# Kernel tuning notes

Hardware: AMD Instinct MI355X
Metric: run time of the kernel (lower is better)

The kernel has to match this reference:

```python
import jax, jax.numpy as jnp
import numpy as np

B, L = 128, 4096
H, RH, D, K = 128, 64, 64, 512  # num_hiddens, residual_hiddens, embedding_dim, num_embeddings
BETA = 0.25  # commitment_cost


def conv1d(x, w, b=None, stride=1, pad=0):
    # x: (N, C, W); w: (O, I, K) torch layout
    y = jax.lax.conv_general_dilated(x, w, (stride,), [(pad, pad)],
                                     dimension_numbers=('NCW', 'OIW', 'NCW'))
    return y if b is None else y + b[None, :, None]


def convT1d(x, w, b=None, stride=2, pad=1):
    # torch ConvTranspose1d weight layout (in, out, k)
    k = w.shape[-1]
    w_t = jnp.flip(w, -1).transpose(1, 0, 2)  # (out, in, k)
    y = jax.lax.conv_general_dilated(x, w_t, (1,), [(k - 1 - pad, k - 1 - pad)],
                                     lhs_dilation=(stride,),
                                     dimension_numbers=('NCW', 'OIW', 'NCW'))
    return y if b is None else y + b[None, :, None]


def res_stack(x, layers):
    for w1, w2 in layers:
        h = conv1d(jax.nn.relu(x), w1, None, 1, 1)
        h = conv1d(jax.nn.relu(h), w2, None, 1, 0)
        x = x + h
    return jax.nn.relu(x)


def _forward(x, enc_w1, enc_b1, enc_w2, enc_b2, enc_w3, enc_b3,
             enc_r1a, enc_r1b, enc_r2a, enc_r2b, pre_vq_w, pre_vq_b, codebook,
             dec_w1, dec_b1, dec_r1a, dec_r1b, dec_r2a, dec_r2b,
             dec_ct1_w, dec_ct1_b, dec_ct2_w, dec_ct2_b):
    # ---- Encoder (compression_factor == 4) ----
    h = x[:, None, :]                                   # (B, 1, L)
    h = jax.nn.relu(conv1d(h, enc_w1, enc_b1, 2, 1))    # (B, H/2, L/2)
    h = jax.nn.relu(conv1d(h, enc_w2, enc_b2, 2, 1))    # (B, H, L/4)
    h = conv1d(h, enc_w3, enc_b3, 1, 1)
    h = res_stack(h, [(enc_r1a, enc_r1b), (enc_r2a, enc_r2b)])
    z = conv1d(h, pre_vq_w, pre_vq_b, 1, 0)             # (B, D, T)

    # ---- Vector quantization ----
    zt = z.transpose(0, 2, 1)                           # (B, T, D)
    flat = zt.reshape(-1, D)                            # (BT, D)
    dists = (jnp.sum(flat * flat, 1, keepdims=True)
             - 2.0 * flat @ codebook.T
             + jnp.sum(codebook * codebook, 1))         # (BT, K)
    idx = jnp.argmin(dists, axis=1)                     # (BT,)
    q = codebook[idx].reshape(zt.shape)                 # (B, T, D)

    e_latent = jnp.mean((jax.lax.stop_gradient(q) - zt) ** 2)
    q_latent = jnp.mean((q - jax.lax.stop_gradient(zt)) ** 2)
    loss = q_latent + BETA * e_latent
    q_st = zt + jax.lax.stop_gradient(q - zt)           # straight-through

    counts = jnp.zeros((K,), flat.dtype).at[idx].add(1.0)
    probs = counts / idx.shape[0]
    perplexity = jnp.exp(-jnp.sum(probs * jnp.log(probs + 1e-10)))

    # ---- Decoder (compression_factor == 4) ----
    hd = q_st.transpose(0, 2, 1)                        # (B, D, T)
    hd = conv1d(hd, dec_w1, dec_b1, 1, 1)               # (B, H, T)
    hd = res_stack(hd, [(dec_r1a, dec_r1b), (dec_r2a, dec_r2b)])
    hd = jax.nn.relu(convT1d(hd, dec_ct1_w, dec_ct1_b)) # (B, H/2, 2T)
    hd = convT1d(hd, dec_ct2_w, dec_ct2_b)              # (B, 1, 4T)
    recon = jnp.squeeze(hd)                             # (B, L)
    return loss, recon, perplexity


def setup_inputs() -> dict:
    key = jax.random.key(0)
    ks = jax.random.split(key, 32)
    n = lambda i, shape, s=0.05: jax.random.normal(ks[i], shape, jnp.float32) * s
    inp = {
        'x': jax.random.normal(ks[0], (B, L), jnp.float32),
        'enc_w1': n(1, (H // 2, 1, 4)), 'enc_b1': jnp.zeros((H // 2,), jnp.float32),
        'enc_w2': n(2, (H, H // 2, 4)), 'enc_b2': jnp.zeros((H,), jnp.float32),
        'enc_w3': n(3, (H, H, 3)), 'enc_b3': jnp.zeros((H,), jnp.float32),
        'enc_r1a': n(4, (RH, H, 3)), 'enc_r1b': n(5, (H, RH, 1)),
        'enc_r2a': n(6, (RH, H, 3)), 'enc_r2b': n(7, (H, RH, 1)),
        'pre_vq_w': n(8, (D, H, 1)), 'pre_vq_b': jnp.zeros((D,), jnp.float32),
        'codebook': jax.random.uniform(ks[9], (K, D), jnp.float32, -1.0 / K, 1.0 / K),
        'dec_w1': n(10, (H, D, 3)), 'dec_b1': jnp.zeros((H,), jnp.float32),
        'dec_r1a': n(11, (RH, H, 3)), 'dec_r1b': n(12, (H, RH, 1)),
        'dec_r2a': n(13, (RH, H, 3)), 'dec_r2b': n(14, (H, RH, 1)),
        'dec_ct1_w': n(15, (H, H // 2, 4)), 'dec_ct1_b': jnp.zeros((H // 2,), jnp.float32),
        'dec_ct2_w': n(16, (H // 2, 1, 4)), 'dec_ct2_b': jnp.zeros((1,), jnp.float32),
    }
    return inp


def reference(x, enc_w1, enc_b1, enc_w2, enc_b2, enc_w3, enc_b3,
              enc_r1a, enc_r1b, enc_r2a, enc_r2b, pre_vq_w, pre_vq_b, codebook,
              dec_w1, dec_b1, dec_r1a, dec_r1b, dec_r2a, dec_r2b,
              dec_ct1_w, dec_ct1_b, dec_ct2_w, dec_ct2_b):
    return _forward(x, enc_w1, enc_b1, enc_w2, enc_b2, enc_w3, enc_b3,
                    enc_r1a, enc_r1b, enc_r2a, enc_r2b, pre_vq_w, pre_vq_b, codebook,
                    dec_w1, dec_b1, dec_r1a, dec_r1b, dec_r2a, dec_r2b,
                    dec_ct1_w, dec_ct1_b, dec_ct2_w, dec_ct2_b)
```

## Files before the change

kernel.cpp:

```cpp
#include <hip/hip_runtime.h>
#include <hip/hip_bf16.h>
#include <math.h>

using bf16 = __hip_bfloat16;
typedef __attribute__((ext_vector_type(4))) float f32x4;
typedef __attribute__((ext_vector_type(8))) short s16x8;

#define MFMA16(a,b,c) __builtin_amdgcn_mfma_f32_16x16x32_bf16((a),(b),(c),0,0,0)


__device__ inline float bf2f(unsigned short u) {
    union { float f; unsigned v; } c; c.v = ((unsigned)u) << 16; return c.f;
}
__device__ inline unsigned short bfbits(float f) {
    union { bf16 h; unsigned short u; } c; c.h = __float2bfloat16(f); return c.u;
}
__device__ inline s16x8 relu8(s16x8 v) {
#pragma unroll
    for (int j = 0; j < 8; ++j)
        v[j] = (short)(((unsigned short)v[j] & 0x8000u) ? 0 : (unsigned short)v[j]);
    return v;
}

__global__ __launch_bounds__(256, 3) void encmid_k(
    const bf16* __restrict__ in, const bf16* __restrict__ w3t,
    const float* __restrict__ b3, const bf16* __restrict__ r1w1,
    const bf16* __restrict__ r1w2, const bf16* __restrict__ r2w1,
    const bf16* __restrict__ r2w2, bf16* __restrict__ out)
{
    __shared__ __align__(16) char smem[47872];
    char* sY = smem;
    char* sX = smem + 21760;
    char* sH = smem + 21760;
    const int tid = threadIdx.x;
    const int b   = blockIdx.y;
    const int l0  = blockIdx.x * 64;
    const bf16* inb = in + (size_t)b * 1024 * 128;

    for (int i = tid; i < 96 * 16; i += 256) {
        int t = i >> 4, c0 = (i & 15) * 8;
        int g = l0 - 16 + t;
        s16x8 v = {};
        if (g >= 0 && g < 1024) v = *(const s16x8*)(inb + (size_t)g * 128 + c0);
        *(s16x8*)(sX + ((t * 136 + c0) << 1)) = v;
    }
    __syncthreads();

    const int lane = tid & 63;
    const int wid  = __builtin_amdgcn_readfirstlane(tid >> 6);
    const int lr   = lane & 15;
    const int kg   = lane >> 4;
    const f32x4 zf4 = {0.f, 0.f, 0.f, 0.f};

    {
        const int co0 = wid * 32;
        f32x4 acc[2][5];
#pragma unroll
        for (int cf = 0; cf < 2; ++cf)
#pragma unroll
            for (int lf = 0; lf < 5; ++lf) acc[cf][lf] = zf4;
#pragma unroll
        for (int k = 0; k < 3; ++k) {
            const bf16* Ab = w3t + (size_t)k * 128 * 128;
#pragma unroll
            for (int ks = 0; ks < 4; ++ks) {
                s16x8 af[2];
#pragma unroll
                for (int cf = 0; cf < 2; ++cf)
                    af[cf] = *(const s16x8*)(Ab + (co0 + cf * 16 + lr) * 128 + ks * 32 + kg * 8);
                s16x8 bfr[5];
#pragma unroll
                for (int lf = 0; lf < 5; ++lf) {
                    int tx = lf * 16 + lr + 7 + k;
                    bfr[lf] = *(const s16x8*)(sX + ((tx * 136 + ks * 32 + kg * 8) << 1));
                }
#pragma unroll
                for (int cf = 0; cf < 2; ++cf)
#pragma unroll
                    for (int lf = 0; lf < 5; ++lf)
                        acc[cf][lf] = MFMA16(af[cf], bfr[lf], acc[cf][lf]);
            }
        }
        __syncthreads();
#pragma unroll
        for (int cf = 0; cf < 2; ++cf)
#pragma unroll
            for (int lf = 0; lf < 5; ++lf) {
                int row = lf * 16 + lr;
                int p   = l0 - 8 + row;
                int cb0 = co0 + cf * 16 + kg * 4;
                bool ok = (p >= 0 && p < 1024);
                float r[4];
#pragma unroll
                for (int j = 0; j < 4; ++j)
                    r[j] = ok ? (acc[cf][lf][j] + b3[cb0 + j]) : 0.f;
                uint2 pk;
                pk.x = (unsigned)bfbits(r[0]) | ((unsigned)bfbits(r[1]) << 16);
                pk.y = (unsigned)bfbits(r[2]) | ((unsigned)bfbits(r[3]) << 16);
                *(uint2*)(sY + ((row * 136 + cb0) << 1)) = pk;
            }
    }
    __syncthreads();

#pragma unroll 1
    for (int blk = 0; blk < 2; ++blk) {
        const bf16* w1 = blk ? r2w1 : r1w1;
        {
            const int co0 = wid * 16;
            f32x4 acc[5];
#pragma unroll
            for (int lf = 0; lf < 5; ++lf) acc[lf] = zf4;
#pragma unroll
            for (int k = 0; k < 3; ++k) {
                const bf16* Ab = w1 + (size_t)k * 64 * 128;
#pragma unroll
                for (int ks = 0; ks < 4; ++ks) {
                    s16x8 a = *(const s16x8*)(Ab + (co0 + lr) * 128 + ks * 32 + kg * 8);
                    s16x8 bfr[5];
#pragma unroll
                    for (int lf = 0; lf < 5; ++lf) {
                        int ry = lf * 16 + lr + k - 1;
                        ry = (ry < 0) ? 0 : (ry > 79 ? 79 : ry);
                        bfr[lf] = relu8(*(const s16x8*)(sY + ((ry * 136 + ks * 32 + kg * 8) << 1)));
                    }
#pragma unroll
                    for (int lf = 0; lf < 5; ++lf)
                        acc[lf] = MFMA16(a, bfr[lf], acc[lf]);
                }
            }
#pragma unroll
            for (int lf = 0; lf < 5; ++lf) {
                int row = lf * 16 + lr;
                int ch0 = co0 + kg * 4;
                uint2 pk;
                pk.x = (unsigned)bfbits(fmaxf(acc[lf][0], 0.f)) |
                       ((unsigned)bfbits(fmaxf(acc[lf][1], 0.f)) << 16);
                pk.y = (unsigned)bfbits(fmaxf(acc[lf][2], 0.f)) |
                       ((unsigned)bfbits(fmaxf(acc[lf][3], 0.f)) << 16);
                *(uint2*)(sH + ((row * 72 + ch0) << 1)) = pk;
            }
        }
        __syncthreads();

        if (blk == 0) {
            const int co0 = wid * 32;
            f32x4 acc[2][5];
#pragma unroll
            for (int cf = 0; cf < 2; ++cf)
#pragma unroll
                for (int lf = 0; lf < 5; ++lf) acc[cf][lf] = zf4;
#pragma unroll
            for (int ks = 0; ks < 2; ++ks) {
                s16x8 af[2];
#pragma unroll
                for (int cf = 0; cf < 2; ++cf)
                    af[cf] = *(const s16x8*)(r1w2 + (size_t)(co0 + cf * 16 + lr) * 64 + ks * 32 + kg * 8);
                s16x8 bfr[5];
#pragma unroll
                for (int lf = 0; lf < 5; ++lf) {
                    int row = lf * 16 + lr;
                    bfr[lf] = *(const s16x8*)(sH + ((row * 72 + ks * 32 + kg * 8) << 1));
                }
#pragma unroll
                for (int cf = 0; cf < 2; ++cf)
#pragma unroll
                    for (int lf = 0; lf < 5; ++lf)
                        acc[cf][lf] = MFMA16(af[cf], bfr[lf], acc[cf][lf]);
            }
#pragma unroll
            for (int cf = 0; cf < 2; ++cf)
#pragma unroll
                for (int lf = 0; lf < 5; ++lf) {
                    int row = lf * 16 + lr;
                    int p   = l0 - 8 + row;
                    int cb0 = co0 + cf * 16 + kg * 4;
                    uint2 old = *(const uint2*)(sY + ((row * 136 + cb0) << 1));
                    bool ok = (p >= 0 && p < 1024);
                    float r[4];
                    r[0] = acc[cf][lf][0] + bf2f((unsigned short)(old.x & 0xffff));
                    r[1] = acc[cf][lf][1] + bf2f((unsigned short)(old.x >> 16));
                    r[2] = acc[cf][lf][2] + bf2f((unsigned short)(old.y & 0xffff));
                    r[3] = acc[cf][lf][3] + bf2f((unsigned short)(old.y >> 16));
                    uint2 pk;
                    pk.x = ok ? ((unsigned)bfbits(r[0]) | ((unsigned)bfbits(r[1]) << 16)) : 0u;
                    pk.y = ok ? ((unsigned)bfbits(r[2]) | ((unsigned)bfbits(r[3]) << 16)) : 0u;
                    *(uint2*)(sY + ((row * 136 + cb0) << 1)) = pk;
                }
            __syncthreads();
        } else {
            const int co0 = wid * 32;
            f32x4 acc[2][4];
#pragma unroll
            for (int cf = 0; cf < 2; ++cf)
#pragma unroll
                for (int lf = 0; lf < 4; ++lf) acc[cf][lf] = zf4;
#pragma unroll
            for (int ks = 0; ks < 2; ++ks) {
                s16x8 af[2];
#pragma unroll
                for (int cf = 0; cf < 2; ++cf)
                    af[cf] = *(const s16x8*)(r2w2 + (size_t)(co0 + cf * 16 + lr) * 64 + ks * 32 + kg * 8);
                s16x8 bfr[4];
#pragma unroll
                for (int lf = 0; lf < 4; ++lf) {
                    int row = 8 + lf * 16 + lr;
                    bfr[lf] = *(const s16x8*)(sH + ((row * 72 + ks * 32 + kg * 8) << 1));
                }
#pragma unroll
                for (int cf = 0; cf < 2; ++cf)
#pragma unroll
                    for (int lf = 0; lf < 4; ++lf)
                        acc[cf][lf] = MFMA16(af[cf], bfr[lf], acc[cf][lf]);
            }
#pragma unroll
            for (int cf = 0; cf < 2; ++cf)
#pragma unroll
                for (int lf = 0; lf < 4; ++lf) {
                    int row = 8 + lf * 16 + lr;
                    int cb0 = co0 + cf * 16 + kg * 4;
                    uint2 old = *(const uint2*)(sY + ((row * 136 + cb0) << 1));
                    float r[4];
                    r[0] = fmaxf(acc[cf][lf][0] + bf2f((unsigned short)(old.x & 0xffff)), 0.f);
                    r[1] = fmaxf(acc[cf][lf][1] + bf2f((unsigned short)(old.x >> 16)), 0.f);
                    r[2] = fmaxf(acc[cf][lf][2] + bf2f((unsigned short)(old.y & 0xffff)), 0.f);
                    r[3] = fmaxf(acc[cf][lf][3] + bf2f((unsigned short)(old.y >> 16)), 0.f);
                    uint2 pk;
                    pk.x = (unsigned)bfbits(r[0]) | ((unsigned)bfbits(r[1]) << 16);
                    pk.y = (unsigned)bfbits(r[2]) | ((unsigned)bfbits(r[3]) << 16);
                    *(uint2*)(out + ((size_t)b * 1024 + l0 + lf * 16 + lr) * 128 + cb0) = pk;
                }
        }
    }
}

__global__ __launch_bounds__(256, 4) void decmid_k(
    const bf16* __restrict__ qin, const bf16* __restrict__ dw1,
    const float* __restrict__ db1, const bf16* __restrict__ r1w1,
    const bf16* __restrict__ r1w2, const bf16* __restrict__ r2w1,
    const bf16* __restrict__ r2w2, const bf16* __restrict__ ct1w,
    const float* __restrict__ ct1b, bf16* __restrict__ out)
{
    __shared__ __align__(16) char smem[35584];
    char* sY = smem;
    char* sQ = smem + 21760;
    char* sH = smem + 21760;
    const int tid = threadIdx.x;
    const int b   = blockIdx.y;
    const int l0  = blockIdx.x * 64;
    const bf16* inb = qin + (size_t)b * 1024 * 64;

    for (int i = tid; i < 96 * 8; i += 256) {
        int t = i >> 3, c0 = (i & 7) * 8;
        int g = l0 - 16 + t;
        s16x8 v = {};
        if (g >= 0 && g < 1024) v = *(const s16x8*)(inb + (size_t)g * 64 + c0);
        *(s16x8*)(sQ + ((t * 72 + c0) << 1)) = v;
    }
    __syncthreads();

    const int lane = tid & 63;
    const int wid  = __builtin_amdgcn_readfirstlane(tid >> 6);
    const int lr   = lane & 15;
    const int kg   = lane >> 4;
    const f32x4 zf4 = {0.f, 0.f, 0.f, 0.f};

    {
        const int co0 = wid * 32;
        f32x4 acc[2][5];
#pragma unroll
        for (int cf = 0; cf < 2; ++cf)
#pragma unroll
            for (int lf = 0; lf < 5; ++lf) acc[cf][lf] = zf4;
#pragma unroll
        for (int k = 0; k < 3; ++k) {
            const bf16* Ab = dw1 + (size_t)k * 128 * 64;
#pragma unroll
            for (int ks = 0; ks < 2; ++ks) {
                s16x8 af[2];
#pragma unroll
                for (int cf = 0; cf < 2; ++cf)
                    af[cf] = *(const s16x8*)(Ab + (co0 + cf * 16 + lr) * 64 + ks * 32 + kg * 8);
                s16x8 bfr[5];
#pragma unroll
                for (int lf = 0; lf < 5; ++lf) {
                    int tx = lf * 16 + lr + 7 + k;
                    bfr[lf] = *(const s16x8*)(sQ + ((tx * 72 + ks * 32 + kg * 8) << 1));
                }
#pragma unroll
                for (int cf = 0; cf < 2; ++cf)
#pragma unroll
                    for (int lf = 0; lf < 5; ++lf)
                        acc[cf][lf] = MFMA16(af[cf], bfr[lf], acc[cf][lf]);
            }
        }
        __syncthreads();
#pragma unroll
        for (int cf = 0; cf < 2; ++cf)
#pragma unroll
            for (int lf = 0; lf < 5; ++lf) {
                int row = lf * 16 + lr;
                int p   = l0 - 8 + row;
                int cb0 = co0 + cf * 16 + kg * 4;
                bool ok = (p >= 0 && p < 1024);
                float r[4];
#pragma unroll
                for (int j = 0; j < 4; ++j)
                    r[j] = ok ? (acc[cf][lf][j] + db1[cb0 + j]) : 0.f;
                uint2 pk;
                pk.x = (unsigned)bfbits(r[0]) | ((unsigned)bfbits(r[1]) << 16);
                pk.y = (unsigned)bfbits(r[2]) | ((unsigned)bfbits(r[3]) << 16);
                *(uint2*)(sY + ((row * 136 + cb0) << 1)) = pk;
            }
    }
    __syncthreads();

#pragma unroll 1
    for (int blk = 0; blk < 2; ++blk) {
        const bf16* w1 = blk ? r2w1 : r1w1;
        const bf16* w2 = blk ? r2w2 : r1w2;
        {
            const int co0 = wid * 16;
            f32x4 acc[5];
#pragma unroll
            for (int lf = 0; lf < 5; ++lf) acc[lf] = zf4;
#pragma unroll
            for (int k = 0; k < 3; ++k) {
                const bf16* Ab = w1 + (size_t)k * 64 * 128;
#pragma unroll
                for (int ks = 0; ks < 4; ++ks) {
                    s16x8 a = *(const s16x8*)(Ab + (co0 + lr) * 128 + ks * 32 + kg * 8);
                    s16x8 bfr[5];
#pragma unroll
                    for (int lf = 0; lf < 5; ++lf) {
                        int ry = lf * 16 + lr + k - 1;
                        ry = (ry < 0) ? 0 : (ry > 79 ? 79 : ry);
                        bfr[lf] = relu8(*(const s16x8*)(sY + ((ry * 136 + ks * 32 + kg * 8) << 1)));
                    }
#pragma unroll
                    for (int lf = 0; lf < 5; ++lf)
                        acc[lf] = MFMA16(a, bfr[lf], acc[lf]);
                }
            }
#pragma unroll
            for (int lf = 0; lf < 5; ++lf) {
                int row = lf * 16 + lr;
                int ch0 = co0 + kg * 4;
                uint2 pk;
                pk.x = (unsigned)bfbits(fmaxf(acc[lf][0], 0.f)) |
                       ((unsigned)bfbits(fmaxf(acc[lf][1], 0.f)) << 16);
                pk.y = (unsigned)bfbits(fmaxf(acc[lf][2], 0.f)) |
                       ((unsigned)bfbits(fmaxf(acc[lf][3], 0.f)) << 16);
                *(uint2*)(sH + ((row * 72 + ch0) << 1)) = pk;
            }
        }
        __syncthreads();
        {
            const int co0 = wid * 32;
            f32x4 acc[2][5];
#pragma unroll
            for (int cf = 0; cf < 2; ++cf)
#pragma unroll
                for (int lf = 0; lf < 5; ++lf) acc[cf][lf] = zf4;
#pragma unroll
            for (int ks = 0; ks < 2; ++ks) {
                s16x8 af[2];
#pragma unroll
                for (int cf = 0; cf < 2; ++cf)
                    af[cf] = *(const s16x8*)(w2 + (size_t)(co0 + cf * 16 + lr) * 64 + ks * 32 + kg * 8);
                s16x8 bfr[5];
#pragma unroll
                for (int lf = 0; lf < 5; ++lf) {
                    int row = lf * 16 + lr;
                    bfr[lf] = *(const s16x8*)(sH + ((row * 72 + ks * 32 + kg * 8) << 1));
                }
#pragma unroll
                for (int cf = 0; cf < 2; ++cf)
#pragma unroll
                    for (int lf = 0; lf < 5; ++lf)
                        acc[cf][lf] = MFMA16(af[cf], bfr[lf], acc[cf][lf]);
            }
#pragma unroll
            for (int cf = 0; cf < 2; ++cf)
#pragma unroll
                for (int lf = 0; lf < 5; ++lf) {
                    int row = lf * 16 + lr;
                    int p   = l0 - 8 + row;
                    int cb0 = co0 + cf * 16 + kg * 4;
                    uint2 old = *(const uint2*)(sY + ((row * 136 + cb0) << 1));
                    bool ok = (p >= 0 && p < 1024);
                    float r[4];
                    r[0] = acc[cf][lf][0] + bf2f((unsigned short)(old.x & 0xffff));
                    r[1] = acc[cf][lf][1] + bf2f((unsigned short)(old.x >> 16));
                    r[2] = acc[cf][lf][2] + bf2f((unsigned short)(old.y & 0xffff));
                    r[3] = acc[cf][lf][3] + bf2f((unsigned short)(old.y >> 16));
                    if (blk == 1)
#pragma unroll
                        for (int j = 0; j < 4; ++j) r[j] = fmaxf(r[j], 0.f);
                    uint2 pk;
                    pk.x = ok ? ((unsigned)bfbits(r[0]) | ((unsigned)bfbits(r[1]) << 16)) : 0u;
                    pk.y = ok ? ((unsigned)bfbits(r[2]) | ((unsigned)bfbits(r[3]) << 16)) : 0u;
                    *(uint2*)(sY + ((row * 136 + cb0) << 1)) = pk;
                }
        }
        __syncthreads();
    }

    {
        const int co0 = (wid & 1) * 32;
        const int mh  = wid >> 1;
        f32x4 acc[2][2][2];
#pragma unroll
        for (int g = 0; g < 2; ++g)
#pragma unroll
            for (int cf = 0; cf < 2; ++cf)
#pragma unroll
                for (int j = 0; j < 2; ++j) acc[g][cf][j] = zf4;
#pragma unroll
        for (int g = 0; g < 2; ++g)
#pragma unroll
            for (int k = 0; k < 2; ++k) {
                const bf16* Ab = ct1w + (size_t)(g * 2 + k) * 64 * 128;
                const int doff = (g == 0) ? (k - 1) : k;
#pragma unroll
                for (int ks = 0; ks < 4; ++ks) {
                    s16x8 af[2];
#pragma unroll
                    for (int cf = 0; cf < 2; ++cf)
                        af[cf] = *(const s16x8*)(Ab + (co0 + cf * 16 + lr) * 128 + ks * 32 + kg * 8);
                    s16x8 bfr[2];
#pragma unroll
                    for (int j = 0; j < 2; ++j) {
                        int ty = 8 + (mh * 2 + j) * 16 + lr + doff;
                        bfr[j] = *(const s16x8*)(sY + ((ty * 136 + ks * 32 + kg * 8) << 1));
                    }
#pragma unroll
                    for (int cf = 0; cf < 2; ++cf)
#pragma unroll
                        for (int j = 0; j < 2; ++j)
                            acc[g][cf][j] = MFMA16(af[cf], bfr[j], acc[g][cf][j]);
                }
            }
#pragma unroll
        for (int g = 0; g < 2; ++g)
#pragma unroll
            for (int cf = 0; cf < 2; ++cf)
#pragma unroll
                for (int j = 0; j < 2; ++j) {
                    int m   = (mh * 2 + j) * 16 + lr;
                    int cb0 = co0 + cf * 16 + kg * 4;
                    float r[4];
#pragma unroll
                    for (int jj = 0; jj < 4; ++jj)
                        r[jj] = fmaxf(acc[g][cf][j][jj] + ct1b[cb0 + jj], 0.f);
                    uint2 pk;
                    pk.x = (unsigned)bfbits(r[0]) | ((unsigned)bfbits(r[1]) << 16);
                    pk.y = (unsigned)bfbits(r[2]) | ((unsigned)bfbits(r[3]) << 16);
                    *(uint2*)(out + ((size_t)b * 2048 + 2 * (l0 + m) + g) * 64 + cb0) = pk;
                }
    }
}

__global__ __launch_bounds__(256) void enc12_k(
    const float* __restrict__ x, const float* __restrict__ w1,
    const float* __restrict__ b1, const bf16* __restrict__ w2t,
    const float* __restrict__ b2, bf16* __restrict__ out)
{
    __shared__ float sXf[268];
    __shared__ float sW1[256];
    __shared__ float sB1[64];
    __shared__ __align__(16) char sX[132 * 144];
    const int tid = threadIdx.x;
    const int b   = blockIdx.y;
    const int l0  = blockIdx.x * 64;
    const float* xb = x + (size_t)b * 4096;

    for (int i = tid; i < 266; i += 256) {
        int g = 4 * l0 - 3 + i;
        sXf[i] = (g >= 0 && g < 4096) ? xb[g] : 0.f;
    }
    if (tid < 256) sW1[tid] = w1[tid];
    if (tid < 64)  sB1[tid] = b1[tid];
    __syncthreads();

    for (int i = tid; i < 132 * 64; i += 256) {
        int t = i >> 6, c = i & 63;
        int p = (t < 66) ? 2 * (l0 + t) : 2 * (l0 + t - 66) - 1;
        float v = 0.f;
        if (p >= 0 && p < 2048) {
            int xi = 2 * p - 4 * l0 + 2;
            float a = sB1[c];
#pragma unroll
            for (int k = 0; k < 4; ++k) a = fmaf(sXf[xi + k], sW1[c * 4 + k], a);
            v = fmaxf(a, 0.f);
        }
        *(bf16*)(sX + ((t * 72 + c) << 1)) = __float2bfloat16(v);
    }
    __syncthreads();

    const int lane = tid & 63;
    const int wid  = __builtin_amdgcn_readfirstlane(tid >> 6);
    const int co0  = wid * 32;
    const int lr   = lane & 15;
    const int kg   = lane >> 4;

    f32x4 acc[2][4];
#pragma unroll
    for (int cf = 0; cf < 2; ++cf)
#pragma unroll
        for (int lf = 0; lf < 4; ++lf) acc[cf][lf] = (f32x4){0.f, 0.f, 0.f, 0.f};

#pragma unroll
    for (int k = 0; k < 4; ++k) {
        const int roff = (k == 0) ? 66 : (k == 1) ? 0 : (k == 2) ? 67 : 1;
        const bf16* Ab = w2t + (size_t)k * 128 * 64;
#pragma unroll
        for (int ks = 0; ks < 2; ++ks) {
            s16x8 af[2];
#pragma unroll
            for (int cf = 0; cf < 2; ++cf)
                af[cf] = *(const s16x8*)(Ab + (co0 + cf * 16 + lr) * 64 + ks * 32 + kg * 8);
            s16x8 bfr[4];
#pragma unroll
            for (int lf = 0; lf < 4; ++lf) {
                int t = roff + lf * 16 + lr;
                bfr[lf] = *(const s16x8*)(sX + ((t * 72 + ks * 32 + kg * 8) << 1));
            }
#pragma unroll
            for (int cf = 0; cf < 2; ++cf)
#pragma unroll
                for (int lf = 0; lf < 4; ++lf)
                    acc[cf][lf] = MFMA16(af[cf], bfr[lf], acc[cf][lf]);
        }
    }

#pragma unroll
    for (int cf = 0; cf < 2; ++cf)
#pragma unroll
        for (int lf = 0; lf < 4; ++lf) {
            int cb0  = co0 + cf * 16 + kg * 4;
            int lcol = lf * 16 + lr;
            float r[4];
#pragma unroll
            for (int j = 0; j < 4; ++j)
                r[j] = fmaxf(acc[cf][lf][j] + b2[cb0 + j], 0.f);
            uint2 pk;
            pk.x = (unsigned)bfbits(r[0]) | ((unsigned)bfbits(r[1]) << 16);
            pk.y = (unsigned)bfbits(r[2]) | ((unsigned)bfbits(r[3]) << 16);
            *(uint2*)(out + ((size_t)b * 1024 + l0 + lcol) * 128 + cb0) = pk;
        }
}

__global__ __launch_bounds__(256) void ct2_k(
    const bf16* __restrict__ in, const float* __restrict__ w,
    const float* __restrict__ bias, float* __restrict__ out)
{
    __shared__ __align__(16) char sX[258 * 144];
    const int tid = threadIdx.x;
    const int b   = blockIdx.y;
    const int m0  = blockIdx.x * 256;
    const bf16* inb = in + (size_t)b * 2048 * 64;
    for (int i = tid; i < 258 * 8; i += 256) {
        int t = i >> 3, c0 = (i & 7) * 8;
        int g = m0 - 1 + t;
        s16x8 v = {};
        if (g >= 0 && g < 2048) v = *(const s16x8*)(inb + (size_t)g * 64 + c0);
        *(s16x8*)(sX + ((t * 72 + c0) << 1)) = v;
    }
    __syncthreads();
    float e = bias[0], o = bias[0];
#pragma unroll
    for (int c0 = 0; c0 < 64; c0 += 8) {
        s16x8 vm1 = *(const s16x8*)(sX + (((tid + 0) * 72 + c0) << 1));
        s16x8 v0  = *(const s16x8*)(sX + (((tid + 1) * 72 + c0) << 1));
        s16x8 vp1 = *(const s16x8*)(sX + (((tid + 2) * 72 + c0) << 1));
#pragma unroll
        for (int j = 0; j < 8; ++j) {
            int ci = c0 + j;
            float xm1 = bf2f((unsigned short)vm1[j]);
            float x0  = bf2f((unsigned short)v0[j]);
            float xp1 = bf2f((unsigned short)vp1[j]);
            e = fmaf(x0,  w[ci * 4 + 1], fmaf(xm1, w[ci * 4 + 3], e));
            o = fmaf(xp1, w[ci * 4 + 0], fmaf(x0,  w[ci * 4 + 2], o));
        }
    }
    int m = m0 + tid;
    out[(size_t)b * 4096 + 2 * m]     = e;
    out[(size_t)b * 4096 + 2 * m + 1] = o;
}

__global__ __launch_bounds__(256) void wx_k(
    const float* ew2, const float* ew3, const float* er1a, const float* er1b,
    const float* er2a, const float* er2b, const float* pvw, const float* dw1,
    const float* dr1a, const float* dr1b, const float* dr2a, const float* dr2b,
    const float* ct1w, bf16* wb)
{
    const int job = blockIdx.x;
    bf16* dst = wb + (size_t)job * 65536;
    const float* src; int CO, CI, K;
    switch (job) {
        case 0:  src = ew2;  CO = 128; CI = 64;  K = 4; break;
        case 1:  src = ew3;  CO = 128; CI = 128; K = 3; break;
// ... 299 lines not shown
```

Before: 357.6 us.

## Repartition MFMA warp tiling to split time rows across waves in encoder/decoder

Each wave now owns a 16-row time slice and computes all output channels for it, plus a split of the extra 16-row halo tile across waves. Before, each wave owned a channel slice across all 80 rows. This changes which operand is reused in registers: the LDS activation fragment is loaded once and reused across eight weight fragments, at the cost of more global/L2 weight fragment loads per wave. The transposed-conv output is staged through LDS and written back with contiguous 16-byte stores, adding a sync. A pack4 helper is factored out.

Measured after the change: 713.8 us. +99.6%, slower.

```diff
diff --git a/kernel.cpp b/kernel.cpp
--- a/kernel.cpp
+++ b/kernel.cpp
@@ -20,6 +20,12 @@
     for (int j = 0; j < 8; ++j)
         v[j] = (short)(((unsigned short)v[j] & 0x8000u) ? 0 : (unsigned short)v[j]);
     return v;
+}
+__device__ inline uint2 pack4(float a, float b, float c, float d) {
+    uint2 p;
+    p.x = (unsigned)bfbits(a) | ((unsigned)bfbits(b) << 16);
+    p.y = (unsigned)bfbits(c) | ((unsigned)bfbits(d) << 16);
+    return p;
 }
 
 __global__ __launch_bounds__(256, 3) void encmid_k(
@@ -53,182 +59,186 @@
     const f32x4 zf4 = {0.f, 0.f, 0.f, 0.f};
 
     {
-        const int co0 = wid * 32;
-        f32x4 acc[2][5];
-#pragma unroll
-        for (int cf = 0; cf < 2; ++cf)
-#pragma unroll
-            for (int lf = 0; lf < 5; ++lf) acc[cf][lf] = zf4;
+        f32x4 accO[8], acc4[2];
+#pragma unroll
+        for (int cf = 0; cf < 8; ++cf) accO[cf] = zf4;
+        acc4[0] = zf4; acc4[1] = zf4;
 #pragma unroll
         for (int k = 0; k < 3; ++k) {
             const bf16* Ab = w3t + (size_t)k * 128 * 128;
 #pragma unroll
             for (int ks = 0; ks < 4; ++ks) {
-                s16x8 af[2];
-#pragma unroll
-                for (int cf = 0; cf < 2; ++cf)
-                    af[cf] = *(const s16x8*)(Ab + (co0 + cf * 16 + lr) * 128 + ks * 32 + kg * 8);
-                s16x8 bfr[5];
-#pragma unroll
-                for (int lf = 0; lf < 5; ++lf) {
-                    int tx = lf * 16 + lr + 7 + k;
-                    bfr[lf] = *(const s16x8*)(sX + ((tx * 136 + ks * 32 + kg * 8) << 1));
-                }
-#pragma unroll
-                for (int cf = 0; cf < 2; ++cf)
-#pragma unroll
-                    for (int lf = 0; lf < 5; ++lf)
-                        acc[cf][lf] = MFMA16(af[cf], bfr[lf], acc[cf][lf]);
-            }
-        }
-        __syncthreads();
-#pragma unroll
-        for (int cf = 0; cf < 2; ++cf)
-#pragma unroll
-            for (int lf = 0; lf < 5; ++lf) {
-                int row = lf * 16 + lr;
-                int p   = l0 - 8 + row;
-                int cb0 = co0 + cf * 16 + kg * 4;
-                bool ok = (p >= 0 && p < 1024);
+                const int cc = ks * 32 + kg * 8;
+                s16x8 af[8];
+#pragma unroll
+                for (int cf = 0; cf < 8; ++cf)
+                    af[cf] = *(const s16x8*)(Ab + (cf * 16 + lr) * 128 + cc);
+                s16x8 a40 = *(const s16x8*)(Ab + ((wid * 2 + 0) * 16 + lr) * 128 + cc);
+                s16x8 a41 = *(const s16x8*)(Ab + ((wid * 2 + 1) * 16 + lr) * 128 + cc);
+                s16x8 b0 = *(const s16x8*)(sX + (((wid * 16 + lr + 7 + k) * 136 + cc) << 1));
+                s16x8 b4 = *(const s16x8*)(sX + (((64 + lr + 7 + k) * 136 + cc) << 1));
+#pragma unroll
+                for (int cf = 0; cf < 8; ++cf)
+                    accO[cf] = MFMA16(af[cf], b0, accO[cf]);
+                acc4[0] = MFMA16(a40, b4, acc4[0]);
+                acc4[1] = MFMA16(a41, b4, acc4[1]);
+            }
+        }
+        {
+            int row = wid * 16 + lr;
+            int p   = l0 - 8 + row;
+            bool ok = (p >= 0 && p < 1024);
+#pragma unroll
+            for (int cf = 0; cf < 8; ++cf) {
+                int ch0 = cf * 16 + kg * 4;
                 float r[4];
 #pragma unroll
                 for (int j = 0; j < 4; ++j)
-                    r[j] = ok ? (acc[cf][lf][j] + b3[cb0 + j]) : 0.f;
-                uint2 pk;
-                pk.x = (unsigned)bfbits(r[0]) | ((unsigned)bfbits(r[1]) << 16);
-                pk.y = (unsigned)bfbits(r[2]) | ((unsigned)bfbits(r[3]) << 16);
-                *(uint2*)(sY + ((row * 136 + cb0) << 1)) = pk;
-            }
+                    r[j] = ok ? (accO[cf][j] + b3[ch0 + j]) : 0.f;
+                *(uint2*)(sY + ((row * 136 + ch0) << 1)) = pack4(r[0], r[1], r[2], r[3]);
+            }
+            int row4 = 64 + lr;
+            bool ok4 = (l0 - 8 + row4 < 1024);
+#pragma unroll
+            for (int c2 = 0; c2 < 2; ++c2) {
+                int ch0 = (wid * 2 + c2) * 16 + kg * 4;
+                float r[4];
+#pragma unroll
+                for (int j = 0; j < 4; ++j)
+                    r[j] = ok4 ? (acc4[c2][j] + b3[ch0 + j]) : 0.f;
+                *(uint2*)(sY + ((row4 * 136 + ch0) << 1)) = pack4(r[0], r[1], r[2], r[3]);
+            }
+        }
     }
     __syncthreads();
 
 #pragma unroll 1
-    for (int blk = 0; blk < 2; ++blk) {
-        const bf16* w1 = blk ? r2w1 : r1w1;
+    for (int blk2 = 0; blk2 < 2; ++blk2) {
+        const bf16* w1 = blk2 ? r2w1 : r1w1;
+        const bf16* w2 = blk2 ? r2w2 : r1w2;
         {
-            const int co0 = wid * 16;
-            f32x4 acc[5];
-#pragma unroll
-            for (int lf = 0; lf < 5; ++lf) acc[lf] = zf4;
+            f32x4 accO[4], acc4;
+#pragma unroll
+            for (int cf = 0; cf < 4; ++cf) accO[cf] = zf4;
+            acc4 = zf4;
 #pragma unroll
             for (int k = 0; k < 3; ++k) {
                 const bf16* Ab = w1 + (size_t)k * 64 * 128;
 #pragma unroll
                 for (int ks = 0; ks < 4; ++ks) {
-                    s16x8 a = *(const s16x8*)(Ab + (co0 + lr) * 128 + ks * 32 + kg * 8);
-                    s16x8 bfr[5];
-#pragma unroll
-                    for (int lf = 0; lf < 5; ++lf) {
-                        int ry = lf * 16 + lr + k - 1;
-                        ry = (ry < 0) ? 0 : (ry > 79 ? 79 : ry);
-                        bfr[lf] = relu8(*(const s16x8*)(sY + ((ry * 136 + ks * 32 + kg * 8) << 1)));
-                    }
-#pragma unroll
-                    for (int lf = 0; lf < 5; ++lf)
-                        acc[lf] = MFMA16(a, bfr[lf], acc[lf]);
+                    const int cc = ks * 32 + kg * 8;
+                    s16x8 af[4];
+#pragma unroll
+                    for (int cf = 0; cf < 4; ++cf)
+                        af[cf] = *(const s16x8*)(Ab + (cf * 16 + lr) * 128 + cc);
+                    s16x8 a4 = *(const s16x8*)(Ab + (wid * 16 + lr) * 128 + cc);
+                    int ry0 = wid * 16 + lr + k - 1;
+                    ry0 = (ry0 < 0) ? 0 : (ry0 > 79 ? 79 : ry0);
+                    int ry4 = 64 + lr + k - 1;
+                    ry4 = (ry4 > 79) ? 79 : ry4;
+                    s16x8 b0 = relu8(*(const s16x8*)(sY + ((ry0 * 136 + cc) << 1)));
+                    s16x8 b4 = relu8(*(const s16x8*)(sY + ((ry4 * 136 + cc) << 1)));
+#pragma unroll
+                    for (int cf = 0; cf < 4; ++cf)
+                        accO[cf] = MFMA16(af[cf], b0, accO[cf]);
+                    acc4 = MFMA16(a4, b4, acc4);
                 }
             }
-#pragma unroll
-            for (int lf = 0; lf < 5; ++lf) {
-                int row = lf * 16 + lr;
-                int ch0 = co0 + kg * 4;
-                uint2 pk;
-                pk.x = (unsigned)bfbits(fmaxf(acc[lf][0], 0.f)) |
-                       ((unsigned)bfbits(fmaxf(acc[lf][1], 0.f)) << 16);
-                pk.y = (unsigned)bfbits(fmaxf(acc[lf][2], 0.f)) |
-                       ((unsigned)bfbits(fmaxf(acc[lf][3], 0.f)) << 16);
-                *(uint2*)(sH + ((row * 72 + ch0) << 1)) = pk;
-            }
+            int row = wid * 16 + lr;
+#pragma unroll
+            for (int cf = 0; cf < 4; ++cf) {
+                int ch0 = cf * 16 + kg * 4;
+                *(uint2*)(sH + ((row * 72 + ch0) << 1)) =
+                    pack4(fmaxf(accO[cf][0], 0.f), fmaxf(accO[cf][1], 0.f),
+                          fmaxf(accO[cf][2], 0.f), fmaxf(accO[cf][3], 0.f));
+            }
+            int row4 = 64 + lr;
+            int ch4 = wid * 16 + kg * 4;
+            *(uint2*)(sH + ((row4 * 72 + ch4) << 1)) =
+                pack4(fmaxf(acc4[0], 0.f), fmaxf(acc4[1], 0.f),
+                      fmaxf(acc4[2], 0.f), fmaxf(acc4[3], 0.f));
         }
         __syncthreads();
 
-        if (blk == 0) {
-            const int co0 = wid * 32;
-            f32x4 acc[2][5];
-#pragma unroll
-            for (int cf = 0; cf < 2; ++cf)
-#pragma unroll
-                for (int lf = 0; lf < 5; ++lf) acc[cf][lf] = zf4;
+        if (blk2 == 0) {
+            f32x4 accO[8], acc4[2];
+#pragma unroll
+            for (int cf = 0; cf < 8; ++cf) accO[cf] = zf4;
+            acc4[0] = zf4; acc4[1] = zf4;
 #pragma unroll
             for (int ks = 0; ks < 2; ++ks) {
-                s16x8 af[2];
-#pragma unroll
-                for (int cf = 0; cf < 2; ++cf)
-                    af[cf] = *(const s16x8*)(r1w2 + (size_t)(co0 + cf * 16 + lr) * 64 + ks * 32 + kg * 8);
-                s16x8 bfr[5];
-#pragma unroll
-                for (int lf = 0; lf < 5; ++lf) {
-                    int row = lf * 16 + lr;
-                    bfr[lf] = *(const s16x8*)(sH + ((row * 72 + ks * 32 + kg * 8) << 1));
-                }
-#pragma unroll
-                for (int cf = 0; cf < 2; ++cf)
-#pragma unroll
-                    for (int lf = 0; lf < 5; ++lf)
-                        acc[cf][lf] = MFMA16(af[cf], bfr[lf], acc[cf][lf]);
-            }
-#pragma unroll
-            for (int cf = 0; cf < 2; ++cf)
-#pragma unroll
-                for (int lf = 0; lf < 5; ++lf) {
-                    int row = lf * 16 + lr;
-                    int p   = l0 - 8 + row;
-                    int cb0 = co0 + cf * 16 + kg * 4;
-                    uint2 old = *(const uint2*)(sY + ((row * 136 + cb0) << 1));
-                    bool ok = (p >= 0 && p < 1024);
-                    float r[4];
-                    r[0] = acc[cf][lf][0] + bf2f((unsigned short)(old.x & 0xffff));
-                    r[1] = acc[cf][lf][1] + bf2f((unsigned short)(old.x >> 16));
-                    r[2] = acc[cf][lf][2] + bf2f((unsigned short)(old.y & 0xffff));
-                    r[3] = acc[cf][lf][3] + bf2f((unsigned short)(old.y >> 16));
-                    uint2 pk;
-                    pk.x = ok ? ((unsigned)bfbits(r[0]) | ((unsigned)bfbits(r[1]) << 16)) : 0u;
-                    pk.y = ok ? ((unsigned)bfbits(r[2]) | ((unsigned)bfbits(r[3]) << 16)) : 0u;
-                    *(uint2*)(sY + ((row * 136 + cb0) << 1)) = pk;
-                }
+                const int cc = ks * 32 + kg * 8;
+                s16x8 af[8];
+#pragma unroll
+                for (int cf = 0; cf < 8; ++cf)
+                    af[cf] = *(const s16x8*)(w2 + (size_t)(cf * 16 + lr) * 64 + cc);
+                s16x8 a40 = *(const s16x8*)(w2 + (size_t)((wid * 2 + 0) * 16 + lr) * 64 + cc);
+                s16x8 a41 = *(const s16x8*)(w2 + (size_t)((wid * 2 + 1) * 16 + lr) * 64 + cc);
+                s16x8 b0 = *(const s16x8*)(sH + (((wid * 16 + lr) * 72 + cc) << 1));
+                s16x8 b4 = *(const s16x8*)(sH + (((64 + lr) * 72 + cc) << 1));
+#pragma unroll
+                for (int cf = 0; cf < 8; ++cf)
+                    accO[cf] = MFMA16(af[cf], b0, accO[cf]);
+                acc4[0] = MFMA16(a40, b4, acc4[0]);
+                acc4[1] = MFMA16(a41, b4, acc4[1]);
+            }
+            int row = wid * 16 + lr;
+            bool ok = (l0 - 8 + row >= 0 && l0 - 8 + row < 1024);
+#pragma unroll
+            for (int cf = 0; cf < 8; ++cf) {
+                int ch0 = cf * 16 + kg * 4;
+                uint2 old = *(const uint2*)(sY + ((row * 136 + ch0) << 1));
+                float r0 = accO[cf][0] + bf2f((unsigned short)(old.x & 0xffff));
+                float r1 = accO[cf][1] + bf2f((unsigned short)(old.x >> 16));
+                float r2 = accO[cf][2] + bf2f((unsigned short)(old.y & 0xffff));
+                float r3 = accO[cf][3] + bf2f((unsigned short)(old.y >> 16));
+                uint2 pk = pack4(r0, r1, r2, r3);
+                if (!ok) { pk.x = 0u; pk.y = 0u; }
+                *(uint2*)(sY + ((row * 136 + ch0) << 1)) = pk;
+            }
+            int row4 = 64 + lr;
+            bool ok4 = (l0 - 8 + row4 < 1024);
+#pragma unroll
+            for (int c2 = 0; c2 < 2; ++c2) {
+                int ch0 = (wid * 2 + c2) * 16 + kg * 4;
+                uint2 old = *(const uint2*)(sY + ((row4 * 136 + ch0) << 1));
+                float r0 = acc4[c2][0] + bf2f((unsigned short)(old.x & 0xffff));
+                float r1 = acc4[c2][1] + bf2f((unsigned short)(old.x >> 16));
+                float r2 = acc4[c2][2] + bf2f((unsigned short)(old.y & 0xffff));
+                float r3 = acc4[c2][3] + bf2f((unsigned short)(old.y >> 16));
+                uint2 pk = pack4(r0, r1, r2, r3);
+                if (!ok4) { pk.x = 0u; pk.y = 0u; }
+                *(uint2*)(sY + ((row4 * 136 + ch0) << 1)) = pk;
+            }
             __syncthreads();
         } else {
-            const int co0 = wid * 32;
-            f32x4 acc[2][4];
-#pragma unroll
-            for (int cf = 0; cf < 2; ++cf)
-#pragma unroll
-                for (int lf = 0; lf < 4; ++lf) acc[cf][lf] = zf4;
+            f32x4 acc[8];
+#pragma unroll
+            for (int cf = 0; cf < 8; ++cf) acc[cf] = zf4;
 #pragma unroll
             for (int ks = 0; ks < 2; ++ks) {
-                s16x8 af[2];
-#pragma unroll
-                for (int cf = 0; cf < 2; ++cf)
-                    af[cf] = *(const s16x8*)(r2w2 + (size_t)(co0 + cf * 16 + lr) * 64 + ks * 32 + kg * 8);
-                s16x8 bfr[4];
-#pragma unroll
-                for (int lf = 0; lf < 4; ++lf) {
-                    int row = 8 + lf * 16 + lr;
-                    bfr[lf] = *(const s16x8*)(sH + ((row * 72 + ks * 32 + kg * 8) << 1));
-                }
-#pragma unroll
-                for (int cf = 0; cf < 2; ++cf)
-#pragma unroll
-                    for (int lf = 0; lf < 4; ++lf)
-                        acc[cf][lf] = MFMA16(af[cf], bfr[lf], acc[cf][lf]);
-            }
-#pragma unroll
-            for (int cf = 0; cf < 2; ++cf)
-#pragma unroll
-                for (int lf = 0; lf < 4; ++lf) {
-                    int row = 8 + lf * 16 + lr;
-                    int cb0 = co0 + cf * 16 + kg * 4;
-                    uint2 old = *(const uint2*)(sY + ((row * 136 + cb0) << 1));
-                    float r[4];
-                    r[0] = fmaxf(acc[cf][lf][0] + bf2f((unsigned short)(old.x & 0xffff)), 0.f);
-                    r[1] = fmaxf(acc[cf][lf][1] + bf2f((unsigned short)(old.x >> 16)), 0.f);
-                    r[2] = fmaxf(acc[cf][lf][2] + bf2f((unsigned short)(old.y & 0xffff)), 0.f);
-                    r[3] = fmaxf(acc[cf][lf][3] + bf2f((unsigned short)(old.y >> 16)), 0.f);
-                    uint2 pk;
-                    pk.x = (unsigned)bfbits(r[0]) | ((unsigned)bfbits(r[1]) << 16);
-                    pk.y = (unsigned)bfbits(r[2]) | ((unsigned)bfbits(r[3]) << 16);
-                    *(uint2*)(out + ((size_t)b * 1024 + l0 + lf * 16 + lr) * 128 + cb0) = pk;
-                }
+                const int cc = ks * 32 + kg * 8;
+                s16x8 af[8];
+#pragma unroll
+                for (int cf = 0; cf < 8; ++cf)
+                    af[cf] = *(const s16x8*)(w2 + (size_t)(cf * 16 + lr) * 64 + cc);
+                s16x8 b0 = *(const s16x8*)(sH + (((8 + wid * 16 + lr) * 72 + cc) << 1));
+#pragma unroll
+                for (int cf = 0; cf < 8; ++cf)
+                    acc[cf] = MFMA16(af[cf], b0, acc[cf]);
+            }
+            int row = 8 + wid * 16 + lr;
+#pragma unroll
+            for (int cf = 0; cf < 8; ++cf) {
+                int ch0 = cf * 16 + kg * 4;
+                uint2 old = *(const uint2*)(sY + ((row * 136 + ch0) << 1));
+                float r0 = fmaxf(acc[cf][0] + bf2f((unsigned short)(old.x & 0xffff)), 0.f);
+                float r1 = fmaxf(acc[cf][1] + bf2f((unsigned short)(old.x >> 16)), 0.f);
+                float r2 = fmaxf(acc[cf][2] + bf2f((unsigned short)(old.y & 0xffff)), 0.f);
+                float r3 = fmaxf(acc[cf][3] + bf2f((unsigned short)(old.y >> 16)), 0.f);
+                *(uint2*)(out + ((size_t)b * 1024 + l0 + wid * 16 + lr) * 128 + ch0) =
+                    pack4(r0, r1, r2, r3);
+            }
         }
     }
 }
@@ -265,156 +275,171 @@
     const f32x4 zf4 = {0.f, 0.f, 0.f, 0.f};
 
     {
-        const int co0 = wid * 32;
-        f32x4 acc[2][5];
-#pragma unroll
-        for (int cf = 0; cf < 2; ++cf)
-#pragma unroll
-            for (int lf = 0; lf < 5; ++lf) acc[cf][lf] = zf4;
+        f32x4 accO[8], acc4[2];
+#pragma unroll
+        for (int cf = 0; cf < 8; ++cf) accO[cf] = zf4;
+        acc4[0] = zf4; acc4[1] = zf4;
 #pragma unroll
         for (int k = 0; k < 3; ++k) {
             const bf16* Ab = dw1 + (size_t)k * 128 * 64;
 #pragma unroll
             for (int ks = 0; ks < 2; ++ks) {
-                s16x8 af[2];
-#pragma unroll
-                for (int cf = 0; cf < 2; ++cf)
-                    af[cf] = *(const s16x8*)(Ab + (co0 + cf * 16 + lr) * 64 + ks * 32 + kg * 8);
-                s16x8 bfr[5];
-#pragma unroll
-                for (int lf = 0; lf < 5; ++lf) {
-                    int tx = lf * 16 + lr + 7 + k;
-                    bfr[lf] = *(const s16x8*)(sQ + ((tx * 72 + ks * 32 + kg * 8) << 1));
-                }
-#pragma unroll
-                for (int cf = 0; cf < 2; ++cf)
-#pragma unroll
-                    for (int lf = 0; lf < 5; ++lf)
-                        acc[cf][lf] = MFMA16(af[cf], bfr[lf], acc[cf][lf]);
-            }
-        }
-        __syncthreads();
-#pragma unroll
-        for (int cf = 0; cf < 2; ++cf)
-#pragma unroll
-            for (int lf = 0; lf < 5; ++lf) {
-                int row = lf * 16 + lr;
-                int p   = l0 - 8 + row;
-                int cb0 = co0 + cf * 16 + kg * 4;
-                bool ok = (p >= 0 && p < 1024);
-                float r[4];
-#pragma unroll
-                for (int j = 0; j < 4; ++j)
-                    r[j] = ok ? (acc[cf][lf][j] + db1[cb0 + j]) : 0.f;
-                uint2 pk;
-                pk.x = (unsigned)bfbits(r[0]) | ((unsigned)bfbits(r[1]) << 16);
-                pk.y = (unsigned)bfbits(r[2]) | ((unsigned)bfbits(r[3]) << 16);
-                *(uint2*)(sY + ((row * 136 + cb0) << 1)) = pk;
-            }
+                const int cc = ks * 32 + kg * 8;
+                s16x8 af[8];
+#pragma unroll
+                for (int cf = 0; cf < 8; ++cf)
+                    af[cf] = *(const s16x8*)(Ab + (cf * 16 + lr) * 64 + cc);
+                s16x8 a40 = *(const s16x8*)(Ab + ((wid * 2 + 0) * 16 + lr) * 64 + cc);
+                s16x8 a41 = *(const s16x8*)(Ab + ((wid * 2 + 1) * 16 + lr) * 64 + cc);
+                s16x8 b0 = *(const s16x8*)(sQ + (((wid * 16 + lr + 7 + k) * 72 + cc) << 1));
+                s16x8 b4 = *(const s16x8*)(sQ + (((64 + lr + 7 + k) * 72 + cc) << 1));
+#pragma unroll
+                for (int cf = 0; cf < 8; ++cf)
+                    accO[cf] = MFMA16(af[cf], b0, accO[cf]);
+                acc4[0] = MFMA16(a40, b4, acc4[0]);
+                acc4[1] = MFMA16(a41, b4, acc4[1]);
+            }
+        }
+        int row = wid * 16 + lr;
+        bool ok = (l0 - 8 + row >= 0 && l0 - 8 + row < 1024);
+#pragma unroll
+        for (int cf = 0; cf < 8; ++cf) {
+            int ch0 = cf * 16 + kg * 4;
+            float r[4];
+#pragma unroll
+            for (int j = 0; j < 4; ++j)
+                r[j] = ok ? (accO[cf][j] + db1[ch0 + j]) : 0.f;
+            *(uint2*)(sY + ((row * 136 + ch0) << 1)) = pack4(r[0], r[1], r[2], r[3]);
+        }
+        int row4 = 64 + lr;
+        bool ok4 = (l0 - 8 + row4 < 1024);
+#pragma unroll
+        for (int c2 = 0; c2 < 2; ++c2) {
+            int ch0 = (wid * 2 + c2) * 16 + kg * 4;
+            float r[4];
+#pragma unroll
+            for (int j = 0; j < 4; ++j)
+                r[j] = ok4 ? (acc4[c2][j] + db1[ch0 + j]) : 0.f;
+            *(uint2*)(sY + ((row4 * 136 + ch0) << 1)) = pack4(r[0], r[1], r[2], r[3]);
+        }
     }
     __syncthreads();
 
 #pragma unroll 1
-    for (int blk = 0; blk < 2; ++blk) {
-        const bf16* w1 = blk ? r2w1 : r1w1;
-        const bf16* w2 = blk ? r2w2 : r1w2;
+    for (int blk2 = 0; blk2 < 2; ++blk2) {
+        const bf16* w1 = blk2 ? r2w1 : r1w1;
+        const bf16* w2 = blk2 ? r2w2 : r1w2;
         {
-            const int co0 = wid * 16;
-            f32x4 acc[5];
-#pragma unroll
-            for (int lf = 0; lf < 5; ++lf) acc[lf] = zf4;
+            f32x4 accO[4], acc4;
+#pragma unroll
+            for (int cf = 0; cf < 4; ++cf) accO[cf] = zf4;
+            acc4 = zf4;
 #pragma unroll
             for (int k = 0; k < 3; ++k) {
                 const bf16* Ab = w1 + (size_t)k * 64 * 128;
 #pragma unroll
                 for (int ks = 0; ks < 4; ++ks) {
-                    s16x8 a = *(const s16x8*)(Ab + (co0 + lr) * 128 + ks * 32 + kg * 8);
-                    s16x8 bfr[5];
-#pragma unroll
-                    for (int lf = 0; lf < 5; ++lf) {
-                        int ry = lf * 16 + lr + k - 1;
-                        ry = (ry < 0) ? 0 : (ry > 79 ? 79 : ry);
-                        bfr[lf] = relu8(*(const s16x8*)(sY + ((ry * 136 + ks * 32 + kg * 8) << 1)));
-                    }
-#pragma unroll
-                    for (int lf = 0; lf < 5; ++lf)
-                        acc[lf] = MFMA16(a, bfr[lf], acc[lf]);
+                    const int cc = ks * 32 + kg * 8;
+                    s16x8 af[4];
+#pragma unroll
+                    for (int cf = 0; cf < 4; ++cf)
+                        af[cf] = *(const s16x8*)(Ab + (cf * 16 + lr) * 128 + cc);
+                    s16x8 a4 = *(const s16x8*)(Ab + (wid * 16 + lr) * 128 + cc);
+                    int ry0 = wid * 16 + lr + k - 1;
+                    ry0 = (ry0 < 0) ? 0 : (ry0 > 79 ? 79 : ry0);
+                    int ry4 = 64 + lr + k - 1;
+                    ry4 = (ry4 > 79) ? 79 : ry4;
+                    s16x8 b0 = relu8(*(const s16x8*)(sY + ((ry0 * 136 + cc) << 1)));
+                    s16x8 b4 = relu8(*(const s16x8*)(sY + ((ry4 * 136 + cc) << 1)));
+#pragma unroll
+                    for (int cf = 0; cf < 4; ++cf)
+                        accO[cf] = MFMA16(af[cf], b0, accO[cf]);
+                    acc4 = MFMA16(a4, b4, acc4);
                 }
             }
-#pragma unroll
-            for (int lf = 0; lf < 5; ++lf) {
-                int row = lf * 16 + lr;
-                int ch0 = co0 + kg * 4;
-                uint2 pk;
-                pk.x = (unsigned)bfbits(fmaxf(acc[lf][0], 0.f)) |
-                       ((unsigned)bfbits(fmaxf(acc[lf][1], 0.f)) << 16);
-                pk.y = (unsigned)bfbits(fmaxf(acc[lf][2], 0.f)) |
-                       ((unsigned)bfbits(fmaxf(acc[lf][3], 0.f)) << 16);
-                *(uint2*)(sH + ((row * 72 + ch0) << 1)) = pk;
-            }
+            int row = wid * 16 + lr;
+#pragma unroll
+            for (int cf = 0; cf < 4; ++cf) {
+                int ch0 = cf * 16 + kg * 4;
+                *(uint2*)(sH + ((row * 72 + ch0) << 1)) =
+                    pack4(fmaxf(accO[cf][0], 0.f), fmaxf(accO[cf][1], 0.f),
+                          fmaxf(accO[cf][2], 0.f), fmaxf(accO[cf][3], 0.f));
+            }
+            int row4 = 64 + lr;
+            int ch4 = wid * 16 + kg * 4;
+            *(uint2*)(sH + ((row4 * 72 + ch4) << 1)) =
+                pack4(fmaxf(acc4[0], 0.f), fmaxf(acc4[1], 0.f),
+                      fmaxf(acc4[2], 0.f), fmaxf(acc4[3], 0.f));
         }
         __syncthreads();
         {
-            const int co0 = wid * 32;
-            f32x4 acc[2][5];
-#pragma unroll
-            for (int cf = 0; cf < 2; ++cf)
-#pragma unroll
-                for (int lf = 0; lf < 5; ++lf) acc[cf][lf] = zf4;
+            f32x4 accO[8], acc4[2];
+#pragma unroll
+            for (int cf = 0; cf < 8; ++cf) accO[cf] = zf4;
+            acc4[0] = zf4; acc4[1] = zf4;
 #pragma unroll
             for (int ks = 0; ks < 2; ++ks) {
-                s16x8 af[2];
-#pragma unroll
-                for (int cf = 0; cf < 2; ++cf)
-                    af[cf] = *(const s16x8*)(w2 + (size_t)(co0 + cf * 16 + lr) * 64 + ks * 32 + kg * 8);
-                s16x8 bfr[5];
-#pragma unroll
-                for (int lf = 0; lf < 5; ++lf) {
-                    int row = lf * 16 + lr;
-                    bfr[lf] = *(const s16x8*)(sH + ((row * 72 + ks * 32 + kg * 8) << 1));
+                const int cc = ks * 32 + kg * 8;
+                s16x8 af[8];
+#pragma unroll
+                for (int cf = 0; cf < 8; ++cf)
+                    af[cf] = *(const s16x8*)(w2 + (size_t)(cf * 16 + lr) * 64 + cc);
+                s16x8 a40 = *(const s16x8*)(w2 + (size_t)((wid * 2 + 0) * 16 + lr) * 64 + cc);
+                s16x8 a41 = *(const s16x8*)(w2 + (size_t)((wid * 2 + 1) * 16 + lr) * 64 + cc);
+                s16x8 b0 = *(const s16x8*)(sH + (((wid * 16 + lr) * 72 + cc) << 1));
+                s16x8 b4 = *(const s16x8*)(sH + (((64 + lr) * 72 + cc) << 1));
+#pragma unroll
+                for (int cf = 0; cf < 8; ++cf)
+                    accO[cf] = MFMA16(af[cf], b0, accO[cf]);
+                acc4[0] = MFMA16(a40, b4, acc4[0]);
+                acc4[1] = MFMA16(a41, b4, acc4[1]);
+            }
+            int row = wid * 16 + lr;
+            bool ok = (l0 - 8 + row >= 0 && l0 - 8 + row < 1024);
+#pragma unroll
+            for (int cf = 0; cf < 8; ++cf) {
+                int ch0 = cf * 16 + kg * 4;
+                uint2 old = *(const uint2*)(sY + ((row * 136 + ch0) << 1));
+                float r0 = accO[cf][0] + bf2f((unsigned short)(old.x & 0xffff));
+                float r1 = accO[cf][1] + bf2f((unsigned short)(old.x >> 16));
+                float r2 = accO[cf][2] + bf2f((unsigned short)(old.y & 0xffff));
+                float r3 = accO[cf][3] + bf2f((unsigned short)(old.y >> 16));
+                if (blk2 == 1) {
+                    r0 = fmaxf(r0, 0.f); r1 = fmaxf(r1, 0.f);
+                    r2 = fmaxf(r2, 0.f); r3 = fmaxf(r3, 0.f);
                 }
-#pragma unroll
-                for (int cf = 0; cf < 2; ++cf)
-#pragma unroll
-                    for (int lf = 0; lf < 5; ++lf)
-                        acc[cf][lf] = MFMA16(af[cf], bfr[lf], acc[cf][lf]);
-            }
-#pragma unroll
-            for (int cf = 0; cf < 2; ++cf)
-#pragma unroll
-                for (int lf = 0; lf < 5; ++lf) {
-                    int row = lf * 16 + lr;
-                    int p   = l0 - 8 + row;
-                    int cb0 = co0 + cf * 16 + kg * 4;
-                    uint2 old = *(const uint2*)(sY + ((row * 136 + cb0) << 1));
-                    bool ok = (p >= 0 && p < 1024);
-                    float r[4];
-                    r[0] = acc[cf][lf][0] + bf2f((unsigned short)(old.x & 0xffff));
-                    r[1] = acc[cf][lf][1] + bf2f((unsigned short)(old.x >> 16));
-                    r[2] = acc[cf][lf][2] + bf2f((unsigned short)(old.y & 0xffff));
-                    r[3] = acc[cf][lf][3] + bf2f((unsigned short)(old.y >> 16));
-                    if (blk == 1)
-#pragma unroll
-                        for (int j = 0; j < 4; ++j) r[j] = fmaxf(r[j], 0.f);
-                    uint2 pk;
-                    pk.x = ok ? ((unsigned)bfbits(r[0]) | ((unsigned)bfbits(r[1]) << 16)) : 0u;
-                    pk.y = ok ? ((unsigned)bfbits(r[2]) | ((unsigned)bfbits(r[3]) << 16)) : 0u;
-                    *(uint2*)(sY + ((row * 136 + cb0) << 1)) = pk;
+                uint2 pk = pack4(r0, r1, r2, r3);
+                if (!ok) { pk.x = 0u; pk.y = 0u; }
+                *(uint2*)(sY + ((row * 136 + ch0) << 1)) = pk;
+            }
+            int row4 = 64 + lr;
+            bool ok4 = (l0 - 8 + row4 < 1024);
+#pragma unroll
+            for (int c2 = 0; c2 < 2; ++c2) {
+                int ch0 = (wid * 2 + c2) * 16 + kg * 4;
+                uint2 old = *(const uint2*)(sY + ((row4 * 136 + ch0) << 1));
+                float r0 = acc4[c2][0] + bf2f((unsigned short)(old.x & 0xffff));
+                float r1 = acc4[c2][1] + bf2f((unsigned short)(old.x >> 16));
+                float r2 = acc4[c2][2] + bf2f((unsigned short)(old.y & 0xffff));
+                float r3 = acc4[c2][3] + bf2f((unsigned short)(old.y >> 16));
+                if (blk2 == 1) {
+                    r0 = fmaxf(r0, 0.f); r1 = fmaxf(r1, 0.f);
+                    r2 = fmaxf(r2, 0.f); r3 = fmaxf(r3, 0.f);
                 }
+                uint2 pk = pack4(r0, r1, r2, r3);
+                if (!ok4) { pk.x = 0u; pk.y = 0u; }
+                *(uint2*)(sY + ((row4 * 136 + ch0) << 1)) = pk;
+            }
         }
         __syncthreads();
     }
 
     {
-        const int co0 = (wid & 1) * 32;
-        const int mh  = wid >> 1;
-        f32x4 acc[2][2][2];
+        f32x4 acc[2][4];
 #pragma unroll
         for (int g = 0; g < 2; ++g)
 #pragma unroll
-            for (int cf = 0; cf < 2; ++cf)
-#pragma unroll
-                for (int j = 0; j < 2; ++j) acc[g][cf][j] = zf4;
+            for (int cf = 0; cf < 4; ++cf) acc[g][cf] = zf4;
 #pragma unroll
         for (int g = 0; g < 2; ++g)
 #pragma unroll
@@ -423,40 +448,37 @@
                 const int doff = (g == 0) ? (k - 1) : k;
 #pragma unroll
                 for (int ks = 0; ks < 4; ++ks) {
-                    s16x8 af[2];
-#pragma unroll
-                    for (int cf = 0; cf < 2; ++cf)
-                        af[cf] = *(const s16x8*)(Ab + (co0 + cf * 16 + lr) * 128 + ks * 32 + kg * 8);
-                    s16x8 bfr[2];
-#pragma unroll
-                    for (int j = 0; j < 2; ++j) {
-                        int ty = 8 + (mh * 2 + j) * 16 + lr + doff;
-                        bfr[j] = *(const s16x8*)(sY + ((ty * 136 + ks * 32 + kg * 8) << 1));
-                    }
-#pragma unroll
-                    for (int cf = 0; cf < 2; ++cf)
-#pragma unroll
-                        for (int j = 0; j < 2; ++j)
-                            acc[g][cf][j] = MFMA16(af[cf], bfr[j], acc[g][cf][j]);
+                    const int cc = ks * 32 + kg * 8;
+                    s16x8 af[4];
+#pragma unroll
+                    for (int cf = 0; cf < 4; ++cf)
+                        af[cf] = *(const s16x8*)(Ab + (cf * 16 + lr) * 128 + cc);
+                    int ty = 8 + wid * 16 + lr + doff;
+                    s16x8 bfr = *(const s16x8*)(sY + ((ty * 136 + cc) << 1));
+#pragma unroll
+                    for (int cf = 0; cf < 4; ++cf)
+                        acc[g][cf] = MFMA16(af[cf], bfr, acc[g][cf]);
                 }
             }
+        __syncthreads();
+
 #pragma unroll
         for (int g = 0; g < 2; ++g)
 #pragma unroll
-            for (int cf = 0; cf < 2; ++cf)
-#pragma unroll
-                for (int j = 0; j < 2; ++j) {
-                    int m   = (mh * 2 + j) * 16 + lr;
-                    int cb0 = co0 + cf * 16 + kg * 4;
-                    float r[4];
-#pragma unroll
-                    for (int jj = 0; jj < 4; ++jj)
-                        r[jj] = fmaxf(acc[g][cf][j][jj] + ct1b[cb0 + jj], 0.f);
-                    uint2 pk;
-                    pk.x = (unsigned)bfbits(r[0]) | ((unsigned)bfbits(r[1]) << 16);
-                    pk.y = (unsigned)bfbits(r[2]) | ((unsigned)bfbits(r[3]) << 16);
-                    *(uint2*)(out + ((size_t)b * 2048 + 2 * (l0 + m) + g) * 64 + cb0) = pk;
-                }
+            for (int cf = 0; cf < 4; ++cf) {
+                int rr  = 2 * (wid * 16 + lr) + g;
+                int ch0 = cf * 16 + kg * 4;
+                float r[4];
+#pragma unroll
+                for (int j = 0; j < 4; ++j)
+                    r[j] = fmaxf(acc[g][cf][j] + ct1b[ch0 + j], 0.f);
+                *(uint2*)(sY + rr * 128 + ch0 * 2) = pack4(r[0], r[1], r[2], r[3]);
+            }
+        __syncthreads();
+
+        bf16* ob = out + ((size_t)b * 2048 + 2 * l0) * 64;
+        for (int i = tid; i < 1024; i += 256)
+            *(s16x8*)(ob + i * 8) = *(const s16x8*)(sY + i * 16);
     }
 }
 
@@ -543,10 +565,8 @@
 #pragma unroll
             for (int j = 0; j < 4; ++j)
                 r[j] = fmaxf(acc[cf][lf][j] + b2[cb0 + j], 0.f);
-            uint2 pk;
-            pk.x = (unsigned)bfbits(r[0]) | ((unsigned)bfbits(r[1]) << 16);
-            pk.y = (unsigned)bfbits(r[2]) | ((unsigned)bfbits(r[3]) << 16);
-            *(uint2*)(out + ((size_t)b * 1024 + l0 + lcol) * 128 + cb0) = pk;
+            *(uint2*)(out + ((size_t)b * 1024 + l0 + lcol) * 128 + cb0) =
+                pack4(r[0], r[1], r[2], r[3]);
         }
 }
 
```
